# Kernel optimization log

Measured on AMD Instinct MI355X. Metric: run time of the kernel, lower is better.

## Reference

```python
import jax, jax.numpy as jnp
import numpy as np


def setup_inputs() -> dict:
    key = jax.random.key(0)
    k1, k2, k3 = jax.random.split(key, 3)
    B, N, D = 4, 4096, 256
    val = jax.random.normal(k1, (B, N, D), dtype=jnp.float32)
    state = jax.random.normal(k2, (B, N), dtype=jnp.float32)
    # val projection weight, scaled for unit-variance outputs
    Wv = jax.random.normal(k3, (D, D), dtype=jnp.float32) / np.sqrt(D)
    return {"val": val, "state": state, "Wv": Wv}


def reference(val, state, Wv):
    # pairwise_fn: dot-product scores over all node pairs -> [B, N, N]
    scores = jnp.einsum("bnd,bmd->bnm", val, val)
    # edge_compress_fn: softsign (non-softmax elementwise nonlinearity)
    edges = scores / (1.0 + jnp.abs(scores))
    # state_proj_fn = identity, val_proj_fn = linear
    projected_state = state                                  # [B, N]
    projected_val = jnp.einsum("bmd,de->bme", val, Wv)       # [B, N, D]
    # dual aggregation reusing the same edge matrix
    delta_state = jnp.einsum("bnm,bm->bn", edges, projected_state)
    delta_val = jnp.einsum("bnm,bmd->bnd", edges, projected_val)
    return (delta_state, delta_val)
```

## Files before the change

### kernel.cpp

```cpp
#include <hip/hip_runtime.h>

typedef unsigned short u16;
typedef unsigned char u8;
typedef unsigned int u32;
typedef __bf16 bf16x8 __attribute__((ext_vector_type(8)));
typedef float  f32x16 __attribute__((ext_vector_type(16)));
typedef int    i32x4  __attribute__((ext_vector_type(4)));
typedef int    i32x16 __attribute__((ext_vector_type(16)));

#define NB 4
#define NN 4096
#define ND 256

#define QPV (127.0f / 4.5f)
#define DPV (4.5f / 16129.0f)
#define QST (127.0f / 4.6f)
#define DST (4.6f / 16129.0f)
#define MAGIC 12582912.0f

__device__ __forceinline__ u16 f2bf(float x) { return __builtin_bit_cast(u16, (__bf16)x); }
__device__ __forceinline__ u32 fbits(float x) { return __builtin_bit_cast(u32, x); }

__device__ __forceinline__ u32 packlow4(float a, float b, float c, float d) {
    u32 p = __builtin_amdgcn_perm(fbits(b), fbits(a), 0x00000400u);
    u32 q = __builtin_amdgcn_perm(fbits(d), fbits(c), 0x00000400u);
    return __builtin_amdgcn_perm(q, p, 0x05040100u);
}



__global__ __launch_bounds__(256) void k_wv(const float* __restrict__ Wv, u16* __restrict__ wv) {
    __shared__ u16 t2[256 * 33];
    int tid = threadIdx.x;
    int es = blockIdx.x, e0 = es * 32;
    #pragma unroll
    for (int k = 0; k < 8; k++) {
        int idx = tid + k * 256;
        int row = idx >> 3, c4 = idx & 7;
        float4 v = *(const float4*)(Wv + row * 256 + e0 + c4 * 4);
        u16* p = t2 + row * 33 + c4 * 4;
        p[0] = f2bf(v.x); p[1] = f2bf(v.y); p[2] = f2bf(v.z); p[3] = f2bf(v.w);
    }
    __syncthreads();
    u16* dst = wv + (size_t)es * 16 * 512;
    #pragma unroll
    for (int k = 0; k < 4; k++) {
        int flat = tid + k * 256;
        int s = flat >> 6, l = flat & 63;
        int l31 = l & 31, h = l >> 5;
        union { u16 o[8]; uint4 q; } u;
        #pragma unroll
        for (int j = 0; j < 8; j++) u.o[j] = t2[(s * 16 + h * 8 + j) * 33 + l31];
        *(uint4*)(dst + (size_t)flat * 8) = u.q;
    }
}

__global__ __launch_bounds__(256) void k_prep(const float* __restrict__ val,
                                              const float* __restrict__ state,
                                              const u16* __restrict__ wvf,
                                              u8* __restrict__ kq8,
                                              float* __restrict__ srow,
                                              u8* __restrict__ vp8) {
    int tid = threadIdx.x;
    int bid = blockIdx.x;
    if (bid < 512) {
        __shared__ float t[32 * 257];
        __shared__ float rmax[32];
        const float* src = val + (size_t)bid * 32 * 256;
        #pragma unroll
        for (int k = 0; k < 8; k++) {
            int idx = tid + k * 256;
            int row = idx >> 6, c4 = idx & 63;
            float4 v = *(const float4*)(src + row * 256 + c4 * 4);
            float* p = t + row * 257 + c4 * 4;
            p[0] = v.x; p[1] = v.y; p[2] = v.z; p[3] = v.w;
        }
        __syncthreads();
        {
            int row = tid >> 3, seg = tid & 7;
            float m = 0.0f;
            #pragma unroll
            for (int i = 0; i < 32; i++) m = fmaxf(m, fabsf(t[row * 257 + seg + i * 8]));
            m = fmaxf(m, __shfl_down(m, 4));
            m = fmaxf(m, __shfl_down(m, 2));
            m = fmaxf(m, __shfl_down(m, 1));
            if (seg == 0) {
                m = fmaxf(m, 1e-20f);
                rmax[row] = m;
                srow[bid * 32 + row] = m * (1.0f / 127.0f);
            }
        }
        __syncthreads();
        u8* dst8 = kq8 + (size_t)bid * 8192;
        #pragma unroll
        for (int k = 0; k < 2; k++) {
            int flat = tid + k * 256;
            int s = flat >> 6, l = flat & 63;
            int l31 = l & 31, h = l >> 5;
            float r127 = 127.0f / rmax[l31];
            const float* p = t + l31 * 257 + s * 32 + h * 16;
            u32 d[4];
            #pragma unroll
            for (int g = 0; g < 4; g++)
                d[g] = packlow4(fmaf(p[4 * g + 0], r127, MAGIC), fmaf(p[4 * g + 1], r127, MAGIC),
                                fmaf(p[4 * g + 2], r127, MAGIC), fmaf(p[4 * g + 3], r127, MAGIC));
            *(uint4*)(dst8 + (size_t)flat * 16) = make_uint4(d[0], d[1], d[2], d[3]);
        }
        {
            int w = tid >> 6, lane = tid & 63;
            int l31 = lane & 31, h = lane >> 5;
            const u16* wv0 = wvf + ((size_t)((w * 2 + 0) * 16)) * 512 + lane * 8;
            const u16* wv1 = wvf + ((size_t)((w * 2 + 1) * 16)) * 512 + lane * 8;
            f32x16 acc0 = {}, acc1 = {};
            for (int s = 0; s < 16; s++) {
                union { u16 o[8]; bf16x8 v; } ua;
                const float* p = t + l31 * 257 + s * 16 + h * 8;
                #pragma unroll
                for (int j = 0; j < 8; j++) ua.o[j] = f2bf(p[j]);
                bf16x8 b0 = *(const bf16x8*)(wv0 + (size_t)s * 512);
                bf16x8 b1 = *(const bf16x8*)(wv1 + (size_t)s * 512);
                acc0 = __builtin_amdgcn_mfma_f32_32x32x16_bf16(ua.v, b0, acc0, 0, 0, 0);
                acc1 = __builtin_amdgcn_mfma_f32_32x32x16_bf16(ua.v, b1, acc1, 0, 0, 0);
            }
            union { u32 wd[4]; i32x4 v; } o0, o1;
            #pragma unroll
            for (int g = 0; g < 4; g++) {
                o0.wd[g] = packlow4(
                    fminf(fmaxf(acc0[4 * g + 0] * QPV, -127.0f), 127.0f) + MAGIC,
                    fminf(fmaxf(acc0[4 * g + 1] * QPV, -127.0f), 127.0f) + MAGIC,
                    fminf(fmaxf(acc0[4 * g + 2] * QPV, -127.0f), 127.0f) + MAGIC,
                    fminf(fmaxf(acc0[4 * g + 3] * QPV, -127.0f), 127.0f) + MAGIC);
                o1.wd[g] = packlow4(
                    fminf(fmaxf(acc1[4 * g + 0] * QPV, -127.0f), 127.0f) + MAGIC,
                    fminf(fmaxf(acc1[4 * g + 1] * QPV, -127.0f), 127.0f) + MAGIC,
                    fminf(fmaxf(acc1[4 * g + 2] * QPV, -127.0f), 127.0f) + MAGIC,
                    fminf(fmaxf(acc1[4 * g + 3] * QPV, -127.0f), 127.0f) + MAGIC);
            }
            *(i32x4*)(vp8 + ((size_t)(bid * 9 + w * 2 + 0)) * 1024 + lane * 16) = o0.v;
            *(i32x4*)(vp8 + ((size_t)(bid * 9 + w * 2 + 1)) * 1024 + lane * 16) = o1.v;
        }
    } else {
        int b = bid - 512;
        __shared__ u8 qs[4096];
        #pragma unroll
        for (int k = 0; k < 16; k++) {
            int i = tid + k * 256;
            float x = fminf(fmaxf(state[b * 4096 + i] * QST, -127.0f), 127.0f);
            qs[i] = (u8)(fbits(x + MAGIC) & 255);
        }
        __syncthreads();
        #pragma unroll
        for (int k = 0; k < 32; k++) {
            int chunk = tid + k * 256;
            int strip = chunk >> 6, lane = chunk & 63, h = (lane >> 5) & 1;
            union { u32 wd[4]; i32x4 v; } u;
            #pragma unroll
            for (int g = 0; g < 4; g++)
                u.wd[g] = *(const u32*)(qs + strip * 32 + 8 * g + 4 * h);
            *(i32x4*)(vp8 + ((size_t)((b * 128 + strip) * 9 + 8)) * 1024 + lane * 16) = u.v;
        }
    }
}

__global__ __launch_bounds__(256, 2) void k_main(const u8* __restrict__ kq8,
                                                 const u8* __restrict__ vp8,
                                                 const float* __restrict__ srow,
                                                 float* __restrict__ ds_out,
                                                 float* __restrict__ dval_out) {
    __shared__ i32x4 pbuf[2][4][64];
    __shared__ int dsqi[4][32];

    int tid = threadIdx.x;
    int w = tid >> 6, lane = tid & 63;
    int l31 = lane & 31, h = lane >> 5;

    int id = blockIdx.x;
    int xcd = id & 7;
    int bb = xcd >> 1;
    int t7 = ((xcd & 1) << 6) | (id >> 3);
    int q0 = t7 * 32;
    size_t bbase = (size_t)bb * 128;

    i32x4 qf[8];
    {
        const u8* qsrc = kq8 + (bbase + t7) * 8192 + lane * 16;
        #pragma unroll
        for (int s = 0; s < 8; s++) qf[s] = *(const i32x4*)(qsrc + (size_t)s * 1024);
    }
    float srq = srow[bb * 4096 + q0 + l31];

    i32x16 oacc[2] = {};
    i32x16 dsa = {};

    i32x4 kf[8], vf[4][2], sf;
    float4 sg[4];
    {
        const u8* kb = kq8 + (bbase + w) * 8192 + lane * 16;
        #pragma unroll
        for (int s = 0; s < 8; s++) kf[s] = *(const i32x4*)(kb + (size_t)s * 1024);
        #pragma unroll
        for (int st = 0; st < 4; st++)
            #pragma unroll
            for (int e = 0; e < 2; e++)
                vf[st][e] = *(const i32x4*)(vp8 + ((size_t)((bbase + st) * 9 + 2 * w + e)) * 1024 + lane * 16);
        sf = *(const i32x4*)(vp8 + ((size_t)((bbase + w) * 9 + 8)) * 1024 + lane * 16);
        const float* srm = srow + bb * 4096 + w * 32;
        #pragma unroll
        for (int g = 0; g < 4; g++) sg[g] = *(const float4*)(srm + g * 8 + h * 4);
    }

    for (int mt = 0; mt < 32; mt++) {
        i32x16 s0 = {}, s1 = {};
        #pragma unroll
        for (int s = 0; s < 8; s += 2) {
            s0 = __builtin_amdgcn_mfma_i32_32x32x32_i8(kf[s], qf[s], s0, 0, 0, 0);
            s1 = __builtin_amdgcn_mfma_i32_32x32x32_i8(kf[s + 1], qf[s + 1], s1, 0, 0, 0);
        }
        if (mt + 1 < 32) {
            const u8* kb = kq8 + (bbase + (mt + 1) * 4 + w) * 8192 + lane * 16;
            #pragma unroll
            for (int s = 0; s < 8; s++) kf[s] = *(const i32x4*)(kb + (size_t)s * 1024);
        }

        float cf[16];
        #pragma unroll
        for (int r = 0; r < 16; r++) {
            float sm = ((const float*)&sg[r >> 2])[r & 3] * srq;
            float xs = (float)(s0[r] + s1[r]) * sm;
            float p = xs * __builtin_amdgcn_rcpf(1.0f + fabsf(xs));
            cf[r] = fmaf(p, 127.0f, MAGIC);
        }
        if (mt + 1 < 32) {
            const float* srm = srow + bb * 4096 + (mt + 1) * 128 + w * 32;
            #pragma unroll
            for (int g = 0; g < 4; g++) sg[g] = *(const float4*)(srm + g * 8 + h * 4);
        }
        union { u32 wd[4]; i32x4 v; } pu;
        pu.wd[0] = packlow4(cf[0], cf[1], cf[2], cf[3]);
        pu.wd[1] = packlow4(cf[4], cf[5], cf[6], cf[7]);
        pu.wd[2] = packlow4(cf[8], cf[9], cf[10], cf[11]);
        pu.wd[3] = packlow4(cf[12], cf[13], cf[14], cf[15]);
        i32x4 pf = pu.v;

        dsa = __builtin_amdgcn_mfma_i32_32x32x32_i8(pf, sf, dsa, 0, 0, 0);
        if (mt + 1 < 32)
            sf = *(const i32x4*)(vp8 + ((size_t)((bbase + (mt + 1) * 4 + w) * 9 + 8)) * 1024 + lane * 16);

        pbuf[mt & 1][w][lane] = pf;
        __syncthreads();
        i32x4 pl[4];
        #pragma unroll
        for (int st = 0; st < 4; st++) pl[st] = pbuf[mt & 1][st][lane];

        #pragma unroll
        for (int st = 0; st < 4; st++) {
            oacc[0] = __builtin_amdgcn_mfma_i32_32x32x32_i8(pl[st], vf[st][0], oacc[0], 0, 0, 0);
            oacc[1] = __builtin_amdgcn_mfma_i32_32x32x32_i8(pl[st], vf[st][1], oacc[1], 0, 0, 0);
        }
        if (mt + 1 < 32) {
            #pragma unroll
            for (int st = 0; st < 4; st++)
                #pragma unroll
                for (int e = 0; e < 2; e++)
                    vf[st][e] = *(const i32x4*)(vp8 + ((size_t)((bbase + (mt + 1) * 4 + st) * 9 + 2 * w + e)) * 1024 + lane * 16);
        }
    }

    if (l31 == 0) {
        #pragma unroll
        for (int r = 0; r < 16; r++) dsqi[w][(r & 3) + 8 * (r >> 2) + 4 * h] = dsa[r];
    }
    #pragma unroll
    for (int e = 0; e < 2; e++) {
        #pragma unroll
        for (int r = 0; r < 16; r++) {
            int row = (r & 3) + 8 * (r >> 2) + 4 * h;
            dval_out[((size_t)(bb * 4096 + q0 + row)) * 256 + (2 * w + e) * 32 + l31] =
                (float)oacc[e][r] * DPV;
        }
    }
    __syncthreads();
    if (w == 0 && lane < 32) {
        int d = dsqi[0][lane] + dsqi[1][lane] + dsqi[2][lane] + dsqi[3][lane];
        ds_out[bb * 4096 + q0 + lane] = (float)d * DST;
    }
}

extern "C" void kernel_launch(void* const* d_in, const int* in_sizes, int n_in,
                              void* d_out, int out_size, void* d_ws, size_t ws_size,
                              hipStream_t stream) {
    const float* val   = (const float*)d_in[0];
    const float* state = (const float*)d_in[1];
    const float* Wv    = (const float*)d_in[2];

    float* ds_out   = (float*)d_out;
    float* dval_out = ds_out + NB * NN;

    u8*  kq8 = (u8*)d_ws;
    u8*  vp8 = kq8 + (size_t)NB * NN * ND;
    u16* wv  = (u16*)(vp8 + (size_t)NB * 128 * 9216);
    float* srow = (float*)(wv + 8 * 16 * 512);

    k_wv<<<8, 256, 0, stream>>>(Wv, wv);
    k_prep<<<516, 256, 0, stream>>>(val, state, wv, kq8, srow, vp8);
    k_main<<<512, 256, 0, stream>>>(kq8, vp8, srow, ds_out, dval_out);
}
```

Baseline: 136.6 us.

## Split main kernel's key dimension in two and add integer reduction pass

Doubles the main grid so each block processes half of the key tiles, writing raw int32 partial accumulators (one half into the output buffer, the other into workspace). A new reduction kernel sums the two partials and applies the dequant scale. The aim is more parallelism and occupancy across CUs for the 512-block launch. The cost is an extra launch plus roughly 16MB of extra global traffic for partial writes and the reduce. It also relies on the workspace being large enough for the new partial buffers.

```diff
diff --git a/kernel.cpp b/kernel.cpp
--- a/kernel.cpp
+++ b/kernel.cpp
@@ -157,7 +157,7 @@
             #pragma unroll
             for (int g = 0; g < 4; g++)
                 u.wd[g] = *(const u32*)(qs + strip * 32 + 8 * g + 4 * h);
-            *(i32x4*)(vp8 + ((size_t)((b * 128 + strip) * 9 + 8)) * 1024 + lane * 16) = u.v;
+            *(i32x4*)(vp8 + ((size_t)((b * 128 + strip) * 9 + 8)) * 1024 + (chunk & 63) * 16) = u.v;
         }
     }
 }
@@ -165,6 +165,8 @@
 __global__ __launch_bounds__(256, 2) void k_main(const u8* __restrict__ kq8,
                                                  const u8* __restrict__ vp8,
                                                  const float* __restrict__ srow,
+                                                 int* __restrict__ pws,
+                                                 int* __restrict__ pds,
                                                  float* __restrict__ ds_out,
                                                  float* __restrict__ dval_out) {
     __shared__ i32x4 pbuf[2][4][64];
@@ -175,11 +177,14 @@
     int l31 = lane & 31, h = lane >> 5;
 
     int id = blockIdx.x;
-    int xcd = id & 7;
+    int half = id >> 9;
+    int idl = id & 511;
+    int xcd = idl & 7;
     int bb = xcd >> 1;
-    int t7 = ((xcd & 1) << 6) | (id >> 3);
+    int t7 = ((xcd & 1) << 6) | (idl >> 3);
     int q0 = t7 * 32;
     size_t bbase = (size_t)bb * 128;
+    int m0 = half * 16, mend = m0 + 16;
 
     i32x4 qf[8];
     {
@@ -195,28 +200,28 @@
     i32x4 kf[8], vf[4][2], sf;
     float4 sg[4];
     {
-        const u8* kb = kq8 + (bbase + w) * 8192 + lane * 16;
+        const u8* kb = kq8 + (bbase + m0 * 4 + w) * 8192 + lane * 16;
         #pragma unroll
         for (int s = 0; s < 8; s++) kf[s] = *(const i32x4*)(kb + (size_t)s * 1024);
         #pragma unroll
         for (int st = 0; st < 4; st++)
             #pragma unroll
             for (int e = 0; e < 2; e++)
-                vf[st][e] = *(const i32x4*)(vp8 + ((size_t)((bbase + st) * 9 + 2 * w + e)) * 1024 + lane * 16);
-        sf = *(const i32x4*)(vp8 + ((size_t)((bbase + w) * 9 + 8)) * 1024 + lane * 16);
-        const float* srm = srow + bb * 4096 + w * 32;
+                vf[st][e] = *(const i32x4*)(vp8 + ((size_t)((bbase + m0 * 4 + st) * 9 + 2 * w + e)) * 1024 + lane * 16);
+        sf = *(const i32x4*)(vp8 + ((size_t)((bbase + m0 * 4 + w) * 9 + 8)) * 1024 + lane * 16);
+        const float* srm = srow + bb * 4096 + m0 * 128 + w * 32;
         #pragma unroll
         for (int g = 0; g < 4; g++) sg[g] = *(const float4*)(srm + g * 8 + h * 4);
     }
 
-    for (int mt = 0; mt < 32; mt++) {
+    for (int mt = m0; mt < mend; mt++) {
         i32x16 s0 = {}, s1 = {};
         #pragma unroll
         for (int s = 0; s < 8; s += 2) {
             s0 = __builtin_amdgcn_mfma_i32_32x32x32_i8(kf[s], qf[s], s0, 0, 0, 0);
             s1 = __builtin_amdgcn_mfma_i32_32x32x32_i8(kf[s + 1], qf[s + 1], s1, 0, 0, 0);
         }
-        if (mt + 1 < 32) {
+        if (mt + 1 < mend) {
             const u8* kb = kq8 + (bbase + (mt + 1) * 4 + w) * 8192 + lane * 16;
             #pragma unroll
             for (int s = 0; s < 8; s++) kf[s] = *(const i32x4*)(kb + (size_t)s * 1024);
@@ -230,7 +235,7 @@
             float p = xs * __builtin_amdgcn_rcpf(1.0f + fabsf(xs));
             cf[r] = fmaf(p, 127.0f, MAGIC);
         }
-        if (mt + 1 < 32) {
+        if (mt + 1 < mend) {
             const float* srm = srow + bb * 4096 + (mt + 1) * 128 + w * 32;
             #pragma unroll
             for (int g = 0; g < 4; g++) sg[g] = *(const float4*)(srm + g * 8 + h * 4);
@@ -243,7 +248,7 @@
         i32x4 pf = pu.v;
 
         dsa = __builtin_amdgcn_mfma_i32_32x32x32_i8(pf, sf, dsa, 0, 0, 0);
-        if (mt + 1 < 32)
+        if (mt + 1 < mend)
             sf = *(const i32x4*)(vp8 + ((size_t)((bbase + (mt + 1) * 4 + w) * 9 + 8)) * 1024 + lane * 16);
 
         pbuf[mt & 1][w][lane] = pf;
@@ -257,7 +262,7 @@
             oacc[0] = __builtin_amdgcn_mfma_i32_32x32x32_i8(pl[st], vf[st][0], oacc[0], 0, 0, 0);
             oacc[1] = __builtin_amdgcn_mfma_i32_32x32x32_i8(pl[st], vf[st][1], oacc[1], 0, 0, 0);
         }
-        if (mt + 1 < 32) {
+        if (mt + 1 < mend) {
             #pragma unroll
             for (int st = 0; st < 4; st++)
                 #pragma unroll
@@ -270,19 +275,54 @@
         #pragma unroll
         for (int r = 0; r < 16; r++) dsqi[w][(r & 3) + 8 * (r >> 2) + 4 * h] = dsa[r];
     }
+    int* outi = (half == 0) ? (int*)dval_out : pws;
     #pragma unroll
     for (int e = 0; e < 2; e++) {
         #pragma unroll
         for (int r = 0; r < 16; r++) {
             int row = (r & 3) + 8 * (r >> 2) + 4 * h;
-            dval_out[((size_t)(bb * 4096 + q0 + row)) * 256 + (2 * w + e) * 32 + l31] =
-                (float)oacc[e][r] * DPV;
+            outi[((size_t)(bb * 4096 + q0 + row)) * 256 + (2 * w + e) * 32 + l31] = oacc[e][r];
         }
     }
     __syncthreads();
     if (w == 0 && lane < 32) {
         int d = dsqi[0][lane] + dsqi[1][lane] + dsqi[2][lane] + dsqi[3][lane];
-        ds_out[bb * 4096 + q0 + lane] = (float)d * DST;
+        int* dsi = (half == 0) ? (int*)ds_out : pds;
+        dsi[bb * 4096 + q0 + lane] = d;
+    }
+}
+
+__global__ __launch_bounds__(256) void k_red(float* __restrict__ ds_out,
+                                             float* __restrict__ dval_out,
+                                             const int* __restrict__ pws,
+                                             const int* __restrict__ pds) {
+    int tid = threadIdx.x;
+    int bid = blockIdx.x;
+    size_t base = (size_t)bid * 8192;
+    int* dv = (int*)dval_out;
+    #pragma unroll
+    for (int k = 0; k < 8; k++) {
+        size_t o = base + (size_t)(tid + k * 256) * 4;
+        i32x4 a = *(const i32x4*)(dv + o);
+        i32x4 b = *(const i32x4*)(pws + o);
+        float4 r;
+        r.x = (float)(a[0] + b[0]) * DPV;
+        r.y = (float)(a[1] + b[1]) * DPV;
+        r.z = (float)(a[2] + b[2]) * DPV;
+        r.w = (float)(a[3] + b[3]) * DPV;
+        *(float4*)(dval_out + o) = r;
+    }
+    if (bid < 16) {
+        size_t o = (size_t)bid * 1024 + (size_t)tid * 4;
+        int* dsv = (int*)ds_out;
+        i32x4 a = *(const i32x4*)(dsv + o);
+        i32x4 b = *(const i32x4*)(pds + o);
+        float4 r;
+        r.x = (float)(a[0] + b[0]) * DST;
+        r.y = (float)(a[1] + b[1]) * DST;
+        r.z = (float)(a[2] + b[2]) * DST;
+        r.w = (float)(a[3] + b[3]) * DST;
+        *(float4*)(ds_out + o) = r;
     }
 }
 
@@ -300,8 +340,11 @@
     u8*  vp8 = kq8 + (size_t)NB * NN * ND;
     u16* wv  = (u16*)(vp8 + (size_t)NB * 128 * 9216);
     float* srow = (float*)(wv + 8 * 16 * 512);
+    int* pws = (int*)(srow + NB * NN);
+    int* pds = pws + (size_t)NB * NN * ND;
 
     k_wv<<<8, 256, 0, stream>>>(Wv, wv);
     k_prep<<<516, 256, 0, stream>>>(val, state, wv, kq8, srow, vp8);
-    k_main<<<512, 256, 0, stream>>>(kq8, vp8, srow, ds_out, dval_out);
-}
+    k_main<<<1024, 256, 0, stream>>>(kq8, vp8, srow, pws, pds, ds_out, dval_out);
+    k_red<<<512, 256, 0, stream>>>(ds_out, dval_out, pws, pds);
+}
```

Result: slower. 153.9 us (+12.6%).

## Drop register prefetch in main loop and raise occupancy to three blocks per CU

Applied to the files above, without the earlier changes.

Removes the software prefetch of next-iteration K, V, state and scale fragments. Each iteration now loads its own operands just before use, which cuts register pressure, so launch bounds go from 2 to 3 blocks per CU. The score MFMA chain also collapses from two interleaved accumulators into one serial accumulator. The aim is to trade explicit in-thread latency hiding for more resident waves, at the risk of exposing load latency and a longer dependent MFMA chain.

```diff
diff --git a/kernel.cpp b/kernel.cpp
--- a/kernel.cpp
+++ b/kernel.cpp
@@ -157,12 +157,12 @@
             #pragma unroll
             for (int g = 0; g < 4; g++)
                 u.wd[g] = *(const u32*)(qs + strip * 32 + 8 * g + 4 * h);
-            *(i32x4*)(vp8 + ((size_t)((b * 128 + strip) * 9 + 8)) * 1024 + lane * 16) = u.v;
-        }
-    }
-}
-
-__global__ __launch_bounds__(256, 2) void k_main(const u8* __restrict__ kq8,
+            *(i32x4*)(vp8 + ((size_t)((b * 128 + strip) * 9 + 8)) * 1024 + (chunk & 63) * 16) = u.v;
+        }
+    }
+}
+
+__global__ __launch_bounds__(256, 3) void k_main(const u8* __restrict__ kq8,
                                                  const u8* __restrict__ vp8,
                                                  const float* __restrict__ srow,
                                                  float* __restrict__ ds_out,
@@ -192,48 +192,29 @@
     i32x16 oacc[2] = {};
     i32x16 dsa = {};
 
-    i32x4 kf[8], vf[4][2], sf;
-    float4 sg[4];
-    {
-        const u8* kb = kq8 + (bbase + w) * 8192 + lane * 16;
+    for (int mt = 0; mt < 32; mt++) {
+        const u8* kb = kq8 + (bbase + mt * 4 + w) * 8192 + lane * 16;
+        i32x4 kf[8];
         #pragma unroll
         for (int s = 0; s < 8; s++) kf[s] = *(const i32x4*)(kb + (size_t)s * 1024);
-        #pragma unroll
-        for (int st = 0; st < 4; st++)
-            #pragma unroll
-            for (int e = 0; e < 2; e++)
-                vf[st][e] = *(const i32x4*)(vp8 + ((size_t)((bbase + st) * 9 + 2 * w + e)) * 1024 + lane * 16);
-        sf = *(const i32x4*)(vp8 + ((size_t)((bbase + w) * 9 + 8)) * 1024 + lane * 16);
-        const float* srm = srow + bb * 4096 + w * 32;
+        const float* srm = srow + bb * 4096 + mt * 128 + w * 32;
+        float4 sg[4];
         #pragma unroll
         for (int g = 0; g < 4; g++) sg[g] = *(const float4*)(srm + g * 8 + h * 4);
-    }
-
-    for (int mt = 0; mt < 32; mt++) {
-        i32x16 s0 = {}, s1 = {};
-        #pragma unroll
-        for (int s = 0; s < 8; s += 2) {
-            s0 = __builtin_amdgcn_mfma_i32_32x32x32_i8(kf[s], qf[s], s0, 0, 0, 0);
-            s1 = __builtin_amdgcn_mfma_i32_32x32x32_i8(kf[s + 1], qf[s + 1], s1, 0, 0, 0);
-        }
-        if (mt + 1 < 32) {
-            const u8* kb = kq8 + (bbase + (mt + 1) * 4 + w) * 8192 + lane * 16;
-            #pragma unroll
-            for (int s = 0; s < 8; s++) kf[s] = *(const i32x4*)(kb + (size_t)s * 1024);
-        }
+        i32x4 sf = *(const i32x4*)(vp8 + ((size_t)((bbase + mt * 4 + w) * 9 + 8)) * 1024 + lane * 16);
+
+        i32x16 sacc = {};
+        #pragma unroll
+        for (int s = 0; s < 8; s++)
+            sacc = __builtin_amdgcn_mfma_i32_32x32x32_i8(kf[s], qf[s], sacc, 0, 0, 0);
 
         float cf[16];
         #pragma unroll
         for (int r = 0; r < 16; r++) {
             float sm = ((const float*)&sg[r >> 2])[r & 3] * srq;
-            float xs = (float)(s0[r] + s1[r]) * sm;
+            float xs = (float)sacc[r] * sm;
             float p = xs * __builtin_amdgcn_rcpf(1.0f + fabsf(xs));
             cf[r] = fmaf(p, 127.0f, MAGIC);
-        }
-        if (mt + 1 < 32) {
-            const float* srm = srow + bb * 4096 + (mt + 1) * 128 + w * 32;
-            #pragma unroll
-            for (int g = 0; g < 4; g++) sg[g] = *(const float4*)(srm + g * 8 + h * 4);
         }
         union { u32 wd[4]; i32x4 v; } pu;
         pu.wd[0] = packlow4(cf[0], cf[1], cf[2], cf[3]);
@@ -243,8 +224,13 @@
         i32x4 pf = pu.v;
 
         dsa = __builtin_amdgcn_mfma_i32_32x32x32_i8(pf, sf, dsa, 0, 0, 0);
-        if (mt + 1 < 32)
-            sf = *(const i32x4*)(vp8 + ((size_t)((bbase + (mt + 1) * 4 + w) * 9 + 8)) * 1024 + lane * 16);
+
+        i32x4 vf[4][2];
+        #pragma unroll
+        for (int st = 0; st < 4; st++)
+            #pragma unroll
+            for (int e = 0; e < 2; e++)
+                vf[st][e] = *(const i32x4*)(vp8 + ((size_t)((bbase + mt * 4 + st) * 9 + 2 * w + e)) * 1024 + lane * 16);
 
         pbuf[mt & 1][w][lane] = pf;
         __syncthreads();
@@ -256,13 +242,6 @@
         for (int st = 0; st < 4; st++) {
             oacc[0] = __builtin_amdgcn_mfma_i32_32x32x32_i8(pl[st], vf[st][0], oacc[0], 0, 0, 0);
             oacc[1] = __builtin_amdgcn_mfma_i32_32x32x32_i8(pl[st], vf[st][1], oacc[1], 0, 0, 0);
-        }
-        if (mt + 1 < 32) {
-            #pragma unroll
-            for (int st = 0; st < 4; st++)
-                #pragma unroll
-                for (int e = 0; e < 2; e++)
-                    vf[st][e] = *(const i32x4*)(vp8 + ((size_t)((bbase + (mt + 1) * 4 + st) * 9 + 2 * w + e)) * 1024 + lane * 16);
         }
     }
 
```

After: 173.3 us. 1.27x slower.
